# Kernel optimization log

Hardware: AMD Instinct MI355X
Metric: run time of the kernel (lower is better)

## Reference

```python
import jax, jax.numpy as jnp
import numpy as np

B, HGRID, WGRID = 4, 32, 32
L = 1 + HGRID * WGRID          # cls token + spatial tokens
INPUT_DIM = 512
HEAD_DIM = 512
N_HEAD = 8
QKV_DIM = HEAD_DIM * N_HEAD    # 4096


def pos_embed_2d(h, w, C, dtype):
    """Standard 2D sinusoidal positional embedding, shape (h*w, C)."""
    d = C // 4
    omega = 1.0 / (10000.0 ** (jnp.arange(d, dtype=jnp.float32) / d))
    ey = jnp.arange(h, dtype=jnp.float32)[:, None] * omega      # (h, d)
    ex = jnp.arange(w, dtype=jnp.float32)[:, None] * omega      # (w, d)
    emb_y = jnp.concatenate([jnp.sin(ey), jnp.cos(ey)], -1)     # (h, 2d)
    emb_x = jnp.concatenate([jnp.sin(ex), jnp.cos(ex)], -1)     # (w, 2d)
    emb = jnp.concatenate([
        jnp.broadcast_to(emb_y[:, None, :], (h, w, 2 * d)),
        jnp.broadcast_to(emb_x[None, :, :], (h, w, 2 * d)),
    ], -1)                                                       # (h, w, C)
    return emb.reshape(h * w, C).astype(dtype)


def setup_inputs() -> dict:
    key = jax.random.key(0)
    ks = jax.random.split(key, 16)
    s = 0.02
    inp = {
        "x": jax.random.normal(ks[0], (B, L, INPUT_DIM), dtype=jnp.float32),
        # Q/K/V linear: weight (out, in) as in torch Linear, bias zeros (per _init_bias)
        "Wq": jax.random.normal(ks[1], (QKV_DIM, INPUT_DIM), jnp.float32) * s,
        "bq": jnp.zeros((QKV_DIM,), jnp.float32),
        "Wk": jax.random.normal(ks[2], (QKV_DIM, INPUT_DIM), jnp.float32) * s,
        "bk": jnp.zeros((QKV_DIM,), jnp.float32),
        "Wv": jax.random.normal(ks[3], (QKV_DIM, INPUT_DIM), jnp.float32) * s,
        "bv": jnp.zeros((QKV_DIM,), jnp.float32),
        # 1x1 conv poolers: weight (out_ch, in_ch) = (HEAD_DIM, HEAD_DIM)
        "Wpq": jax.random.normal(ks[4], (HEAD_DIM, HEAD_DIM), jnp.float32) * s,
        "bpq": jax.random.normal(ks[5], (HEAD_DIM,), jnp.float32) * s,
        "Wpk": jax.random.normal(ks[6], (HEAD_DIM, HEAD_DIM), jnp.float32) * s,
        "bpk": jax.random.normal(ks[7], (HEAD_DIM,), jnp.float32) * s,
        "Wpv": jax.random.normal(ks[8], (HEAD_DIM, HEAD_DIM), jnp.float32) * s,
        "bpv": jax.random.normal(ks[9], (HEAD_DIM,), jnp.float32) * s,
        # dispatcher linear: (INPUT_DIM, QKV_DIM)
        "Wd": jax.random.normal(ks[10], (INPUT_DIM, QKV_DIM), jnp.float32) * s,
        "bd": jax.random.normal(ks[11], (INPUT_DIM,), jnp.float32) * s,
        "h": HGRID,
        "w": WGRID,
    }
    return inp


def _pool(t, Wp, bp):
    """AttentionPooler with kernel=1/stride=1: pointwise conv on spatial tokens,
    cls token passed through unchanged. t: (B, n_head, L, head_dim)."""
    cls_tok = t[:, :, :1, :]
    sp = jnp.einsum('bnlc,oc->bnlo', t[:, :, 1:, :], Wp) + bp
    return jnp.concatenate([cls_tok, sp], axis=2)


def reference(x, Wq, bq, Wk, bk, Wv, bv, Wpq, bpq, Wpk, bpk, Wpv, bpv, Wd, bd, h, w):
    Bs, Ls, _ = x.shape

    def proj(Wt, bt):
        y = jnp.einsum('bli,oi->blo', x, Wt) + bt
        return y.reshape(Bs, Ls, N_HEAD, HEAD_DIM).transpose(0, 2, 1, 3)  # (B,nh,L,hd)

    Q = proj(Wq, bq)
    K = proj(Wk, bk)
    V = proj(Wv, bv)

    PQ = _pool(Q, Wpq, bpq)
    PK = _pool(K, Wpk, bpk)
    PV = _pool(V, Wpv, bpv)

    # relative positional encoding added to pooled Q's spatial tokens
    emb = pos_embed_2d(h, w, HEAD_DIM, PQ.dtype)                 # (h*w, hd)
    PQ = jnp.concatenate([PQ[:, :, :1, :], PQ[:, :, 1:, :] + emb], axis=2)

    scale = 1.0 / jnp.sqrt(jnp.asarray(HEAD_DIM, PQ.dtype))
    logits = jnp.einsum('bnqc,bnkc->bnqk', PQ, PK) * scale
    attn = jax.nn.softmax(logits, axis=-1)
    sa = jnp.einsum('bnqk,bnkc->bnqc', attn, PV)

    # skip connection on spatial tokens only (cls row excluded)
    sa = jnp.concatenate([sa[:, :, :1, :], sa[:, :, 1:, :] + Q[:, :, 1:, :]], axis=2)

    stacked = sa.transpose(0, 2, 1, 3).reshape(Bs, Ls, QKV_DIM)
    out = jnp.einsum('blq,oq->blo', stacked, Wd) + bd
    return out
```

## Files before the change

### kernel.cpp

```cpp
#include <hip/hip_runtime.h>


typedef unsigned short u16;
typedef __attribute__((ext_vector_type(8))) short short8;
typedef __attribute__((ext_vector_type(4))) float floatx4;
typedef __attribute__((ext_vector_type(4))) unsigned short us4;

__device__ __forceinline__ u16 f2bf(float f) {
  union { float f; unsigned u; } x; x.f = f;
  unsigned r = (x.u + 0x7fffu + ((x.u >> 16) & 1u)) >> 16;
  return (u16)r;
}
__device__ __forceinline__ float bf2f(u16 u) {
  union { unsigned u; float f; } x; x.u = ((unsigned)u) << 16;
  return x.f;
}

__device__ __forceinline__ void gld_lds16(const void* g, void* l) {
  __builtin_amdgcn_global_load_lds(
      (const __attribute__((address_space(1))) void*)g,
      (__attribute__((address_space(3))) void*)l, 16, 0, 0);
}

struct CvtArgs { const float* src[8]; u16* dst[8]; int n4[8]; };

__global__ __launch_bounds__(256) void cvt_all(CvtArgs a, int total4, float* __restrict__ e) {
  int t = blockIdx.x * 256 + threadIdx.x;
  if (t >= total4) {
    int et = (t - total4) * 4;
    if (et >= 1024 * 512) return;
#pragma unroll
    for (int u = 0; u < 4; ++u) {
      int idx = et + u;
      int c = idx & 511, sp = idx >> 9;
      int y = sp >> 5, xg = sp & 31;
      int j = c & 127, seg = c >> 7;
      float omega = expf(-(float)j * (9.210340371976184f / 128.f));
      float arg = (float)((seg < 2) ? y : xg) * omega;
      e[idx] = (seg & 1) ? cosf(arg) : sinf(arg);
    }
    return;
  }
#pragma unroll
  for (int s = 0; s < 8; ++s) {
    if (t < a.n4[s]) {
      const float* sp = a.src[s] + (long)t * 4;
      u16* dp = a.dst[s] + (long)t * 4;
      float4 v = *(const float4*)sp;
      dp[0] = f2bf(v.x); dp[1] = f2bf(v.y); dp[2] = f2bf(v.z); dp[3] = f2bf(v.w);
      return;
    }
    t -= a.n4[s];
  }
}

struct CF {
  const u16* W;
  const u16* Wp;
  const u16* xb;
  const float *bq, *bk, *bv, *bpq, *bpk, *bpv;
  u16 *PQ, *PK, *PVt;
  float* bc;
};

__global__ __launch_bounds__(256) void cls_fold(CF a) {
  int wid = blockIdx.x * 4 + (threadIdx.x >> 6);
  int lane = threadIdx.x & 63;
  if (wid < 12288) {
    int mat = wid >> 12, o2 = wid & 4095, n = o2 >> 9, ch = o2 & 511;
    short8 wv = *(const short8*)(a.W + (long)wid * 512 + lane * 8);
    float wf[8];
#pragma unroll
    for (int e = 0; e < 8; ++e) wf[e] = bf2f((u16)wv[e]);
    float ac[4] = {0.f, 0.f, 0.f, 0.f};
#pragma unroll
    for (int b = 0; b < 4; ++b) {
      short8 xv = *(const short8*)(a.xb + ((long)b * 1025) * 512 + lane * 8);
#pragma unroll
      for (int e = 0; e < 8; ++e) ac[b] += wf[e] * bf2f((u16)xv[e]);
    }
#pragma unroll
    for (int o = 32; o > 0; o >>= 1)
#pragma unroll
      for (int b = 0; b < 4; ++b) ac[b] += __shfl_xor(ac[b], o, 64);
    if (lane == 0) {
      const float* bsrc = (mat == 0) ? a.bq : (mat == 1) ? a.bk : a.bv;
      float bias = bsrc[o2];
#pragma unroll
      for (int b = 0; b < 4; ++b) {
        long bn = b * 8 + n;
        u16 v = f2bf(ac[b] + bias);
        if (mat == 0)      a.PQ[(bn * 1025 + 1024) * 512 + ch] = v;
        else if (mat == 1) a.PK[(bn * 1025 + 1024) * 512 + ch] = v;
        else               a.PVt[(bn * 512 + ch) * 1088 + 1024] = v;
      }
    }
  } else {
    int t2 = wid - 12288;
    int mat = t2 >> 12, o2 = t2 & 4095, n = o2 >> 9, o = o2 & 511;
    const float* bsrc = (mat == 0) ? a.bq : (mat == 1) ? a.bk : a.bv;
    short8 wp = *(const short8*)(a.Wp + (long)mat * 262144 + o * 512 + lane * 8);
    const float* bb = bsrc + n * 512 + lane * 8;
    float4 b0 = *(const float4*)bb;
    float4 b1 = *(const float4*)(bb + 4);
    float bf8[8] = {b0.x, b0.y, b0.z, b0.w, b1.x, b1.y, b1.z, b1.w};
    float s = 0.f;
#pragma unroll
    for (int e = 0; e < 8; ++e) s += bf2f((u16)wp[e]) * bf8[e];
#pragma unroll
    for (int o1 = 32; o1 > 0; o1 >>= 1) s += __shfl_xor(s, o1, 64);
    if (lane == 0) {
      const float* bpp = (mat == 0) ? a.bpq : (mat == 1) ? a.bpk : a.bpv;
      a.bc[t2] = s + bpp[o];
    }
  }
}

__global__ __launch_bounds__(256) void s_edge(const u16* __restrict__ PQ,
                                              const u16* __restrict__ PK,
                                              u16* __restrict__ S, int nh) {
  int flat = blockIdx.x;
  int head, seg;
  if (nh == 32) {
    int xcd = flat & 7, s = flat >> 3;
    head = xcd + 8 * (s >> 3);
    seg = s & 7;
  } else {
    head = flat >> 3;
    seg = flat & 7;
  }
  const u16* pq = PQ + (long)head * 1025 * 512;
  const u16* pk = PK + (long)head * 1025 * 512;
  u16* sh = S + (long)head * 1025 * 1088;
#pragma unroll
  for (int i = 0; i < 2; ++i) {
    int local = i * 256 + (int)threadIdx.x;
    if (local >= 257) continue;
    int e = seg * 257 + local;
    if (e >= 2049) continue;
    int q, kv;
    if (e < 1025) { q = 1024; kv = e; }
    else { q = e - 1025; kv = 1024; }
    const u16* a = pq + (long)q * 512;
    const u16* b = pk + (long)kv * 512;
    float acc = 0.f;
    for (int k8 = 0; k8 < 64; ++k8) {
      short8 av = *(const short8*)(a + k8 * 8);
      short8 bv = *(const short8*)(b + k8 * 8);
#pragma unroll
      for (int u = 0; u < 8; ++u) acc += bf2f((u16)av[u]) * bf2f((u16)bv[u]);
    }
    sh[(long)q * 1088 + kv] = f2bf(acc * 0.04419417382415922f);
  }
}

__global__ __launch_bounds__(256) void softmax_rows(u16* __restrict__ S) {
  int flat = blockIdx.x;
  int xcd = flat & 7, s0 = flat >> 3;
  int zi = s0 / 257, blk = s0 - zi * 257;
  int head = xcd + 8 * zi;
  int wv = threadIdx.x >> 6, lane = threadIdx.x & 63;
  int row_i = blk * 4 + wv;
  if (row_i > 1024) return;
  u16* row = S + ((long)head * 1025 + row_i) * 1088;
  float v[16];
  float mx = -1e30f;
#pragma unroll
  for (int i = 0; i < 4; ++i) {
    us4 p = *(const us4*)(row + i * 256 + lane * 4);
#pragma unroll
    for (int e = 0; e < 4; ++e) { v[i * 4 + e] = bf2f(p[e]); mx = fmaxf(mx, v[i * 4 + e]); }
  }
  float e1024 = (lane == 0) ? bf2f(row[1024]) : -1e30f;
  mx = fmaxf(mx, e1024);
  for (int o = 32; o > 0; o >>= 1) mx = fmaxf(mx, __shfl_xor(mx, o, 64));
  float s = 0.f;
#pragma unroll
  for (int i = 0; i < 16; ++i) { v[i] = __expf(v[i] - mx); s += v[i]; }
  e1024 = (lane == 0) ? __expf(e1024 - mx) : 0.f;
  s += e1024;
  for (int o = 32; o > 0; o >>= 1) s += __shfl_xor(s, o, 64);
  float inv = 1.0f / s;
#pragma unroll
  for (int i = 0; i < 4; ++i) {
    us4 q;
#pragma unroll
    for (int e = 0; e < 4; ++e) q[e] = f2bf(v[i * 4 + e] * inv);
    *(us4*)(row + i * 256 + lane * 4) = q;
  }
  if (lane < 16) {
    us4 q;
#pragma unroll
    for (int e = 0; e < 4; ++e) q[e] = 0;
    if (lane == 0) q[0] = f2bf(e1024 * inv);
    *(us4*)(row + 1024 + lane * 4) = q;
  }
}

__global__ __launch_bounds__(256) void reduce2(const float* __restrict__ part,
                                               const float* __restrict__ bd,
                                               float* __restrict__ out) {
  int t = blockIdx.x * 256 + threadIdx.x;
  long i = (long)t * 4;
  const long STR = 4100ll * 512;
  float4 a = *(const float4*)(part + i);
  float4 b = *(const float4*)(part + i + STR);
  float4 bb = *(const float4*)(bd + (int)(i & 511));
  float4 r;
  r.x = a.x + b.x + bb.x;
  r.y = a.y + b.y + bb.y;
  r.z = a.z + b.z + bb.z;
  r.w = a.w + b.w + bb.w;
  *(float4*)(out + i) = r;
}

struct GP {
  const u16* A; const u16* A2; const u16* B; const u16* B2;
  const float* c0; const float* c1; const float* c2;
  const float* emb; const u16* resid;
  u16* o0; u16* o1; u16* o2;
  u16* p0; u16* p1; u16* p2;
  float* of; int bz0;
};

template <int MODE>
__global__ __launch_bounds__(256) void gemm_bt(GP g) {
  constexpr int KLEN = (MODE == 5) ? 2048 : ((MODE == 4) ? 1088 : 512);
  constexpr int KITER = KLEN / 64;
  __shared__ u16 smem[16384];
  u16* As = smem;
  u16* Bs = smem + 8192;
  const int tid = threadIdx.x;
  const int lane = tid & 63;
  const int wv = tid >> 6;
  const int wr = wv >> 1, wc = wv & 1;
  const int ccol = lane & 15;
  const int rgrp = lane >> 4;

  int mt, nt, bz, mh = 0;
  if constexpr (MODE == 3 || MODE == 4) {
    constexpr int PER = (MODE == 3) ? 64 : 36;
    constexpr int NTW = (MODE == 3) ? 8 : 4;
    int flat = blockIdx.x;
    int xcd = flat & 7, s = flat >> 3;
    bz = xcd + 8 * (s / PER);
    int tile = s % PER;
    mt = tile / NTW;
    nt = tile % NTW;
  } else if constexpr (MODE == 2) {
    int flat = blockIdx.x;
    int xcd = flat & 7, s = flat >> 3;
    bz = 0;
    mt = xcd * 4 + (s >> 5);
    nt = s & 31;
  } else if constexpr (MODE == 6) {
    int flat = blockIdx.x;
    mh = flat >> 4;
    int tile = flat & 15;
    mt = tile >> 2; nt = tile & 3; bz = 0;
  } else {
    mt = blockIdx.y; nt = blockIdx.x; bz = blockIdx.z;
  }
  const int gbz = g.bz0 + bz;

  const u16* Ap = g.A;
  const u16* Bp = g.B;
  if constexpr (MODE == 0) {
    if (nt >= 64) Bp = g.B2;
  }

  int a_row[4], b_row[4], kx[4];
#pragma unroll
  for (int c = 0; c < 4; ++c) {
    int idx = c * 256 + tid;
    int row = idx >> 3;
    kx[c] = ((idx & 7) ^ (row & 7)) * 8;
    {
      int r = mt * 128 + row;
      int off;
      if constexpr (MODE == 0 || MODE == 2) { off = ((r >> 10) * 1025 + 1 + (r & 1023)) * 512; }
      else if constexpr (MODE == 3) { off = gbz * (1025 * 512) + r * 512; }
      else if constexpr (MODE == 4) { r = r < 1024 ? r : 1024; off = bz * (1025 * 1088) + r * 1088; }
      else if constexpr (MODE == 6) { off = (mh >> 3) * 262144 + r * 512; }
      else { r = r < 4099 ? r : 4099; off = r * 4096; }
      a_row[c] = off;
    }
    {
      int off;
      if constexpr (MODE == 6) {
        int rb = idx >> 4, s2 = idx & 15;
        int cg = (s2 - ((rb >> 3) << 1)) & 15;
        off = mh * 262144 + rb * 512 + nt * 128 + cg * 8;
      } else {
        int r = nt * 128 + row;
        if constexpr (MODE == 0) { off = ((nt >= 64) ? (r - 8192) : r) * 512; }
        else if constexpr (MODE == 3) { off = gbz * (1025 * 512) + r * 512; }
        else if constexpr (MODE == 4) { off = gbz * (512 * 1088) + r * 1088; }
        else if constexpr (MODE == 5) { off = r * 4096; }
        else { off = r * 512; }
      }
      b_row[c] = off;
    }
  }

  floatx4 acc[4][4];
  {
    float binit[4] = {0.f, 0.f, 0.f, 0.f};
    if constexpr (MODE == 0) {
      int sec = nt >> 5;
      const float* bs = (sec < 2) ? (g.c0 + sec * 4096) : g.c1;
#pragma unroll
      for (int j = 0; j < 4; ++j) binit[j] = bs[(nt & 31) * 128 + wc * 64 + j * 16 + ccol];
    }
    if constexpr (MODE == 2) {
#pragma unroll
      for (int j = 0; j < 4; ++j) binit[j] = g.c0[nt * 128 + wc * 64 + j * 16 + ccol];
    }
#pragma unroll
    for (int i = 0; i < 4; ++i)
#pragma unroll
      for (int j = 0; j < 4; ++j)
#pragma unroll
        for (int rr = 0; rr < 4; ++rr) acc[i][j][rr] = binit[j];
  }

  const int kbase = (MODE == 5) ? bz * 2048 : 0;
  const int l15 = lane & 15;
  const int lq = lane >> 4;
  const int l7 = lane & 7;

  for (int kt = 0; kt < KITER; ++kt) {
    const int k0 = kbase + kt * 64;
#pragma unroll
    for (int c = 0; c < 4; ++c)
      gld_lds16(Ap + a_row[c] + k0 + kx[c], (char*)As + (c * 256 + wv * 64) * 16);
#pragma unroll
    for (int c = 0; c < 4; ++c) {
      if constexpr (MODE == 6)
        gld_lds16(Bp + b_row[c] + k0 * 512, (char*)Bs + (c * 256 + wv * 64) * 16);
      else
        gld_lds16(Bp + b_row[c] + k0 + kx[c], (char*)Bs + (c * 256 + wv * 64) * 16);
    }
    __syncthreads();
#pragma unroll
    for (int ks = 0; ks < 2; ++ks) {
      const int ch = ((ks * 4 + lq) ^ l7) * 8;
      short8 af[4], bfr[4];
#pragma unroll
      for (int i = 0; i < 4; ++i)
        af[i] = *(const short8*)(As + (wr * 64 + i * 16 + l15) * 64 + ch);
      if constexpr (MODE == 6) {
#pragma unroll
        for (int j = 0; j < 4; ++j) {
          int ro = ((wc * 64 + j * 16 + l15) + ((ks * 4 + lq) << 4)) & 127;
          const u16* bp2 = Bs + (ks * 32 + lq * 8) * 128 + ro;
          short8 tv;
#pragma unroll
          for (int e = 0; e < 8; ++e) tv[e] = (short)bp2[e * 128];
          bfr[j] = tv;
        }
      } else {
#pragma unroll
        for (int j = 0; j < 4; ++j)
          bfr[j] = *(const short8*)(Bs + (wc * 64 + j * 16 + l15) * 64 + ch);
      }
#pragma unroll
      for (int i = 0; i < 4; ++i)
#pragma unroll
        for (int j = 0; j < 4; ++j)
          acc[i][j] = __builtin_amdgcn_mfma_f32_16x16x32_bf16(af[i], bfr[j], acc[i][j], 0, 0, 0);
    }
    __syncthreads();
  }

  if constexpr (MODE == 2) {
#pragma unroll
    for (int i = 0; i < 4; ++i)
#pragma unroll
      for (int j = 0; j < 4; ++j)
#pragma unroll
        for (int rr = 0; rr < 4; ++rr) {
          int lr2 = wc * 64 + j * 16 + ccol;
          int lc2 = wr * 64 + i * 16 + rgrp * 4 + rr;
          smem[lr2 * 128 + (lc2 ^ ((lr2 & 15) << 3))] = f2bf(acc[i][j][rr]);
        }
    __syncthreads();
    {
      int b = mt >> 3, sp0 = (mt & 7) * 128;
      int n = nt >> 2, ch0 = (nt & 3) * 128;
      long bn = b * 8 + n;
#pragma unroll
      for (int q = 0; q < 8; ++q) {
        int cid = q * 256 + tid;
        int r = cid >> 4;
        int c = cid & 15;
        int pc = c ^ (r & 15);
        short8 val = *(const short8*)(smem + r * 128 + pc * 8);
        *(short8*)(g.o0 + (bn * 512 + ch0 + r) * 1088 + sp0 + c * 8) = val;
      }
    }
  } else if constexpr (MODE == 0 || MODE == 3 || MODE == 4 || MODE == 6) {
#pragma unroll
    for (int i = 0; i < 4; ++i)
#pragma unroll
      for (int j = 0; j < 4; ++j)
#pragma unroll
        for (int rr = 0; rr < 4; ++rr) {
          int lr = wr * 64 + i * 16 + rgrp * 4 + rr;
          int lc = wc * 64 + j * 16 + ccol;
          float v = acc[i][j][rr];
          if constexpr (MODE == 3) v *= 0.04419417382415922f;
          smem[lr * 128 + (lc ^ (rgrp << 4))] = f2bf(v);
        }
    __syncthreads();
#pragma unroll
    for (int q = 0; q < 8; ++q) {
      int cid = q * 256 + tid;
      int r = cid >> 4;
      int c = cid & 15;
      int pc = c ^ ((((unsigned)r >> 2) & 3) << 1);
      short8 val = *(const short8*)(smem + r * 128 + pc * 8);
      int grow = mt * 128 + r;
      if constexpr (MODE == 0) {
        const int sec = nt >> 5;
        int b = grow >> 10, sp = grow & 1023;
        int gcol = (nt & 31) * 128 + c * 8;
        int n = gcol >> 9, ch2 = gcol & 511;
        long bn = b * 8 + n;
        if (sec == 0) {
          const float* ep = g.emb + sp * 512 + ch2;
          float4 e0 = *(const float4*)ep;
          float4 e1 = *(const float4*)(ep + 4);
          float ee[8] = {e0.x, e0.y, e0.z, e0.w, e1.x, e1.y, e1.z, e1.w};
          short8 outv;
#pragma unroll
          for (int e = 0; e < 8; ++e) outv[e] = (short)f2bf(bf2f((u16)val[e]) + ee[e]);
          *(short8*)(g.o0 + (bn * 1025 + sp) * 512 + ch2) = outv;
        } else if (sec == 1) {
          *(short8*)(g.o1 + (bn * 1025 + sp) * 512 + ch2) = val;
        } else {
          *(short8*)(g.o2 + (bn * 1025 + 1 + sp) * 512 + ch2) = val;
        }
      } else if constexpr (MODE == 3) {
        *(short8*)(g.o0 + ((long)bz * 1025 + grow) * 1088 + nt * 128 + c * 8) = val;
      } else if constexpr (MODE == 6) {
        *(short8*)(g.o0 + ((long)(mh * 512) + grow) * 512 + nt * 128 + c * 8) = val;
      } else {
        if (grow <= 1024) {
          int gcol0 = nt * 128 + c * 8;
          short8 outv = val;
          int l = (grow == 1024) ? 0 : grow + 1;
          if (grow < 1024) {
            short8 rs = *(const short8*)(g.resid + ((long)gbz * 1025 + l) * 512 + gcol0);
#pragma unroll
            for (int e = 0; e < 8; ++e)
              outv[e] = (short)f2bf(bf2f((u16)val[e]) + bf2f((u16)rs[e]));
          }
          int b = gbz >> 3, n = gbz & 7;
          *(short8*)(g.o0 + (((long)b * 1025 + l) * 8 + n) * 512 + gcol0) = outv;
        }
      }
    }
  } else {
#pragma unroll
    for (int i = 0; i < 4; ++i) {
#pragma unroll
      for (int j = 0; j < 4; ++j) {
        const int gcol = nt * 128 + wc * 64 + j * 16 + ccol;
#pragma unroll
        for (int rr = 0; rr < 4; ++rr) {
          const int grow = mt * 128 + wr * 64 + i * 16 + rgrp * 4 + rr;
          if (grow < 4100)
            g.of[((long)bz * 4100 + grow) * 512 + gcol] = acc[i][j][rr];
        }
      }
    }
  }
}

extern "C" void kernel_launch(void* const* d_in, const int* in_sizes, int n_in,
                              void* d_out, int out_size, void* d_ws, size_t ws_size,
                              hipStream_t stream) {
  const float* x   = (const float*)d_in[0];
  const float* Wq  = (const float*)d_in[1];
  const float* bq  = (const float*)d_in[2];
  const float* Wk  = (const float*)d_in[3];
  const float* bk  = (const float*)d_in[4];
  const float* Wv  = (const float*)d_in[5];
  const float* bv  = (const float*)d_in[6];
  const float* Wpq = (const float*)d_in[7];
  const float* bpq = (const float*)d_in[8];
  const float* Wpk = (const float*)d_in[9];
  const float* bpk = (const float*)d_in[10];
  const float* Wpv = (const float*)d_in[11];
  const float* bpv = (const float*)d_in[12];
  const float* Wd  = (const float*)d_in[13];
  const float* bd  = (const float*)d_in[14];
  float* out = (float*)d_out;

  char* ws = (char*)d_ws;
  size_t off = 0;
  auto alloc = [&](size_t bytes) {
    char* p = ws + off;
    off += (bytes + 255) & ~(size_t)255;
    return p;
  };
  u16* Wpqb = (u16*)alloc(512ull * 512 * 2);
  u16* Wpkb = (u16*)alloc(512ull * 512 * 2);
  u16* Wpvb = (u16*)alloc(512ull * 512 * 2);
  u16* Wdb  = (u16*)alloc(4096ull * 512 * 2);
  u16* Q    = (u16*)alloc(32ull * 1025 * 512 * 2);
  u16* PQ   = (u16*)alloc(32ull * 1025 * 512 * 2);
  u16* PK   = (u16*)alloc(32ull * 1025 * 512 * 2);
  u16* PVt  = (u16*)alloc(32ull * 512 * 1088 * 2);
  size_t s_off = off;
  u16* xb   = (u16*)alloc(4100ull * 512 * 2);
  u16* Wqb  = (u16*)alloc(4096ull * 512 * 2);
  u16* Wkb  = (u16*)alloc(4096ull * 512 * 2);
  u16* Wvb  = (u16*)alloc(4096ull * 512 * 2);
  u16* Wc   = (u16*)alloc(3ull * 4096 * 512 * 2);
  float* bc = (float*)alloc(3ull * 4096 * 4);
  float* embp = (float*)alloc(1024ull * 512 * 4);
  size_t fixed_need = off;
  u16* S = (u16*)(ws + s_off);
  float* part = (float*)PQ;
  (void)in_sizes; (void)n_in; (void)out_size; (void)Wkb; (void)Wvb;
  (void)Wpkb; (void)Wpvb;

  const size_t sbytes = 1025ull * 1088 * 2;
  size_t need1 = s_off + 32ull * sbytes;
  size_t need2 = s_off + 16ull * sbytes;
  size_t stk4_off = s_off + ((8ull * sbytes + 255) & ~(size_t)255);
  size_t need4 = stk4_off + 4100ull * 4096 * 2;
  int nchunk;
  u16* stk;
  if (ws_size >= need1)      { nchunk = 1; stk = PK; }
  else if (ws_size >= need2 && ws_size >= fixed_need) { nchunk = 2; stk = PK; }
  else if (ws_size >= need4 && ws_size >= fixed_need) {
    nchunk = 4; stk = (u16*)(ws + stk4_off);
  } else return;
  if (nchunk == 2) {
    size_t stk2_off = s_off + ((16ull * sbytes + 255) & ~(size_t)255);
    if (ws_size >= stk2_off + 4100ull * 4096 * 2) stk = (u16*)(ws + stk2_off);
    else {
      nchunk = 4;
      if (ws_size >= need4) stk = (u16*)(ws + stk4_off);
      else return;
    }
  }
  int hpc = 32 / nchunk;

  CvtArgs ca;
  ca.src[0] = x;   ca.dst[0] = xb;   ca.n4[0] = 4100 * 512 / 4;
  ca.src[1] = Wq;  ca.dst[1] = Wqb;  ca.n4[1] = 4096 * 512 / 4;
  ca.src[2] = Wk;  ca.dst[2] = Wkb;  ca.n4[2] = 4096 * 512 / 4;
  ca.src[3] = Wv;  ca.dst[3] = Wvb;  ca.n4[3] = 4096 * 512 / 4;
  ca.src[4] = Wpq; ca.dst[4] = Wpqb; ca.n4[4] = 512 * 512 / 4;
  ca.src[5] = Wpk; ca.dst[5] = Wpkb; ca.n4[5] = 512 * 512 / 4;
  ca.src[6] = Wpv; ca.dst[6] = Wpvb; ca.n4[6] = 512 * 512 / 4;
  ca.src[7] = Wd;  ca.dst[7] = Wdb;  ca.n4[7] = 512 * 4096 / 4;
  int total4 = 0;
  for (int s = 0; s < 8; ++s) total4 += ca.n4[s];
  int grid1 = (total4 + 1024 * 512 / 4 + 255) / 256;
  cvt_all<<<grid1, 256, 0, stream>>>(ca, total4, embp);

  {
    GP g = {};
    g.A = Wpqb; g.B = Wqb; g.o0 = Wc;
    gemm_bt<6><<<dim3(384, 1, 1), 256, 0, stream>>>(g);
  }
  {
    CF cf;
    cf.W = Wqb; cf.Wp = Wpqb; cf.xb = xb;
    cf.bq = bq; cf.bk = bk; cf.bv = bv;
    cf.bpq = bpq; cf.bpk = bpk; cf.bpv = bpv;
    cf.PQ = PQ; cf.PK = PK; cf.PVt = PVt; cf.bc = bc;
    cls_fold<<<6144, 256, 0, stream>>>(cf);
  }

  {
    GP g = {};
    g.A = xb; g.B = Wc; g.B2 = Wqb;
    g.c0 = bc; g.c1 = bq; g.emb = embp;
    g.o0 = PQ; g.o1 = PK; g.o2 = Q;
    gemm_bt<0><<<dim3(96, 32, 1), 256, 0, stream>>>(g);
  }
  {
    GP g = {};
    g.A = xb; g.B = Wc + 8192 * 512; g.c0 = bc + 8192; g.o0 = PVt;
    gemm_bt<2><<<dim3(1024, 1, 1), 256, 0, stream>>>(g);
  }

  for (int c = 0; c < nchunk; ++c) {
    GP g3 = {}; g3.A = PQ; g3.B = PK; g3.o0 = S; g3.bz0 = c * hpc;
    gemm_bt<3><<<dim3(64 * hpc, 1, 1), 256, 0, stream>>>(g3);
    s_edge<<<hpc * 8, 256, 0, stream>>>(
        PQ + (long)c * hpc * 1025 * 512, PK + (long)c * hpc * 1025 * 512, S, hpc);
    softmax_rows<<<257 * hpc, 256, 0, stream>>>(S);
    GP g4 = {}; g4.A = S; g4.B = PVt; g4.resid = Q; g4.o0 = stk; g4.bz0 = c * hpc;
    gemm_bt<4><<<dim3(36 * hpc, 1, 1), 256, 0, stream>>>(g4);
  }

  {
    GP g = {}; g.A = stk; g.B = Wdb; g.of = part;
    gemm_bt<5><<<dim3(4, 33, 2), 256, 0, stream>>>(g);
  }
  reduce2<<<(4100 * 512 / 4 + 255) / 256, 256, 0, stream>>>(part, bd, out);
}
```

Measured before the change: 429.1 us.

## Fold Q skip connection through dispatcher weight as precomputed x·(Wd·Wq) term

Instead of materialising Q (B×8×1025×512) in the projection GEMM and adding it as a residual in the attention-output GEMM, the skip term is folded algebraically: Wd·Wq is precomputed as a 512×512 matrix and multiplied directly with x. A bias term Wd·bq is also folded into the final bias for spatial rows. This removes a third of the projection GEMM output writes and the residual reads, at the cost of a small extra GEMM, an fp32 residual buffer, and a different rounding path. The final K-split also changes from 2 to 4 partial sums, so the reduction kernel reads four partials.

Result: slower. 505.6 us (+17.8%).

```diff
diff --git a/kernel.cpp b/kernel.cpp
--- a/kernel.cpp
+++ b/kernel.cpp
@@ -57,10 +57,12 @@
 struct CF {
   const u16* W;
   const u16* Wp;
+  const u16* Wdbp;
   const u16* xb;
-  const float *bq, *bk, *bv, *bpq, *bpk, *bpv;
+  const float *bq, *bk, *bv, *bpq, *bpk, *bpv, *bd;
   u16 *PQ, *PK, *PVt;
   float* bc;
+  float* bdq;
 };
 
 __global__ __launch_bounds__(256) void cls_fold(CF a) {
@@ -95,7 +97,7 @@
         else               a.PVt[(bn * 512 + ch) * 1088 + 1024] = v;
       }
     }
-  } else {
+  } else if (wid < 24576) {
     int t2 = wid - 12288;
     int mat = t2 >> 12, o2 = t2 & 4095, n = o2 >> 9, o = o2 & 511;
     const float* bsrc = (mat == 0) ? a.bq : (mat == 1) ? a.bk : a.bv;
@@ -113,6 +115,21 @@
       const float* bpp = (mat == 0) ? a.bpq : (mat == 1) ? a.bpk : a.bpv;
       a.bc[t2] = s + bpp[o];
     }
+  } else {
+    int o = wid - 24576;
+    float s = 0.f;
+    for (int c8 = 0; c8 < 8; ++c8) {
+      int base = c8 * 512 + lane * 8;
+      short8 wv = *(const short8*)(a.Wdbp + (long)o * 4096 + base);
+      float4 b0 = *(const float4*)(a.bq + base);
+      float4 b1 = *(const float4*)(a.bq + base + 4);
+      float bf8[8] = {b0.x, b0.y, b0.z, b0.w, b1.x, b1.y, b1.z, b1.w};
+#pragma unroll
+      for (int e = 0; e < 8; ++e) s += bf2f((u16)wv[e]) * bf8[e];
+    }
+#pragma unroll
+    for (int o1 = 32; o1 > 0; o1 >>= 1) s += __shfl_xor(s, o1, 64);
+    if (lane == 0) a.bdq[o] = a.bd[o] + s;
   }
 }
 
@@ -197,20 +214,35 @@
   }
 }
 
-__global__ __launch_bounds__(256) void reduce2(const float* __restrict__ part,
+__global__ __launch_bounds__(256) void reduce3(const float* __restrict__ part,
+                                               const float* __restrict__ xres,
                                                const float* __restrict__ bd,
+                                               const float* __restrict__ bdq,
                                                float* __restrict__ out) {
   int t = blockIdx.x * 256 + threadIdx.x;
   long i = (long)t * 4;
   const long STR = 4100ll * 512;
-  float4 a = *(const float4*)(part + i);
-  float4 b = *(const float4*)(part + i + STR);
-  float4 bb = *(const float4*)(bd + (int)(i & 511));
+  float4 a0 = *(const float4*)(part + i);
+  float4 a1 = *(const float4*)(part + i + STR);
+  float4 a2 = *(const float4*)(part + i + 2 * STR);
+  float4 a3 = *(const float4*)(part + i + 3 * STR);
+  int row = (int)(i >> 9);
+  int l = row % 1025;
+  int ch = (int)(i & 511);
   float4 r;
-  r.x = a.x + b.x + bb.x;
-  r.y = a.y + b.y + bb.y;
-  r.z = a.z + b.z + bb.z;
-  r.w = a.w + b.w + bb.w;
+  r.x = a0.x + a1.x + a2.x + a3.x;
+  r.y = a0.y + a1.y + a2.y + a3.y;
+  r.z = a0.z + a1.z + a2.z + a3.z;
+  r.w = a0.w + a1.w + a2.w + a3.w;
+  if (l > 0) {
+    float4 xr = *(const float4*)(xres + i);
+    float4 bb = *(const float4*)(bdq + ch);
+    r.x += xr.x + bb.x; r.y += xr.y + bb.y;
+    r.z += xr.z + bb.z; r.w += xr.w + bb.w;
+  } else {
+    float4 bb = *(const float4*)(bd + ch);
+    r.x += bb.x; r.y += bb.y; r.z += bb.z; r.w += bb.w;
+  }
   *(float4*)(out + i) = r;
 }
 
@@ -225,7 +257,7 @@
 
 template <int MODE>
 __global__ __launch_bounds__(256) void gemm_bt(GP g) {
-  constexpr int KLEN = (MODE == 5) ? 2048 : ((MODE == 4) ? 1088 : 512);
+  constexpr int KLEN = (MODE == 5) ? 1024 : ((MODE == 4) ? 1088 : ((MODE == 7) ? 4096 : 512));
   constexpr int KITER = KLEN / 64;
   __shared__ u16 smem[16384];
   u16* As = smem;
@@ -258,6 +290,8 @@
     mh = flat >> 4;
     int tile = flat & 15;
     mt = tile >> 2; nt = tile & 3; bz = 0;
+  } else if constexpr (MODE == 7 || MODE == 8) {
+    mt = blockIdx.x >> 2; nt = blockIdx.x & 3; bz = 0;
   } else {
     mt = blockIdx.y; nt = blockIdx.x; bz = blockIdx.z;
   }
@@ -265,9 +299,6 @@
 
   const u16* Ap = g.A;
   const u16* Bp = g.B;
-  if constexpr (MODE == 0) {
-    if (nt >= 64) Bp = g.B2;
-  }
 
   int a_row[4], b_row[4], kx[4];
 #pragma unroll
@@ -278,23 +309,23 @@
     {
       int r = mt * 128 + row;
       int off;
-      if constexpr (MODE == 0 || MODE == 2) { off = ((r >> 10) * 1025 + 1 + (r & 1023)) * 512; }
+      if constexpr (MODE == 0 || MODE == 2 || MODE == 8) { off = ((r >> 10) * 1025 + 1 + (r & 1023)) * 512; }
       else if constexpr (MODE == 3) { off = gbz * (1025 * 512) + r * 512; }
       else if constexpr (MODE == 4) { r = r < 1024 ? r : 1024; off = bz * (1025 * 1088) + r * 1088; }
       else if constexpr (MODE == 6) { off = (mh >> 3) * 262144 + r * 512; }
+      else if constexpr (MODE == 7) { off = r * 4096; }
       else { r = r < 4099 ? r : 4099; off = r * 4096; }
       a_row[c] = off;
     }
     {
       int off;
-      if constexpr (MODE == 6) {
+      if constexpr (MODE == 6 || MODE == 7) {
         int rb = idx >> 4, s2 = idx & 15;
         int cg = (s2 - ((rb >> 3) << 1)) & 15;
-        off = mh * 262144 + rb * 512 + nt * 128 + cg * 8;
+        off = ((MODE == 6) ? mh * 262144 : 0) + rb * 512 + nt * 128 + cg * 8;
       } else {
         int r = nt * 128 + row;
-        if constexpr (MODE == 0) { off = ((nt >= 64) ? (r - 8192) : r) * 512; }
-        else if constexpr (MODE == 3) { off = gbz * (1025 * 512) + r * 512; }
+        if constexpr (MODE == 3) { off = gbz * (1025 * 512) + r * 512; }
         else if constexpr (MODE == 4) { off = gbz * (512 * 1088) + r * 1088; }
         else if constexpr (MODE == 5) { off = r * 4096; }
         else { off = r * 512; }
@@ -308,7 +339,7 @@
     float binit[4] = {0.f, 0.f, 0.f, 0.f};
     if constexpr (MODE == 0) {
       int sec = nt >> 5;
-      const float* bs = (sec < 2) ? (g.c0 + sec * 4096) : g.c1;
+      const float* bs = g.c0 + sec * 4096;
 #pragma unroll
       for (int j = 0; j < 4; ++j) binit[j] = bs[(nt & 31) * 128 + wc * 64 + j * 16 + ccol];
     }
@@ -324,7 +355,7 @@
         for (int rr = 0; rr < 4; ++rr) acc[i][j][rr] = binit[j];
   }
 
-  const int kbase = (MODE == 5) ? bz * 2048 : 0;
+  const int kbase = (MODE == 5) ? bz * 1024 : 0;
   const int l15 = lane & 15;
   const int lq = lane >> 4;
   const int l7 = lane & 7;
@@ -336,7 +367,7 @@
       gld_lds16(Ap + a_row[c] + k0 + kx[c], (char*)As + (c * 256 + wv * 64) * 16);
 #pragma unroll
     for (int c = 0; c < 4; ++c) {
-      if constexpr (MODE == 6)
+      if constexpr (MODE == 6 || MODE == 7)
         gld_lds16(Bp + b_row[c] + k0 * 512, (char*)Bs + (c * 256 + wv * 64) * 16);
       else
         gld_lds16(Bp + b_row[c] + k0 + kx[c], (char*)Bs + (c * 256 + wv * 64) * 16);
@@ -349,7 +380,7 @@
 #pragma unroll
       for (int i = 0; i < 4; ++i)
         af[i] = *(const short8*)(As + (wr * 64 + i * 16 + l15) * 64 + ch);
-      if constexpr (MODE == 6) {
+      if constexpr (MODE == 6 || MODE == 7) {
 #pragma unroll
         for (int j = 0; j < 4; ++j) {
           int ro = ((wc * 64 + j * 16 + l15) + ((ks * 4 + lq) << 4)) & 127;
@@ -399,7 +430,7 @@
         *(short8*)(g.o0 + (bn * 512 + ch0 + r) * 1088 + sp0 + c * 8) = val;
       }
     }
-  } else if constexpr (MODE == 0 || MODE == 3 || MODE == 4 || MODE == 6) {
+  } else if constexpr (MODE == 0 || MODE == 3 || MODE == 4 || MODE == 6 || MODE == 7) {
 #pragma unroll
     for (int i = 0; i < 4; ++i)
 #pragma unroll
@@ -436,28 +467,33 @@
 #pragma unroll
           for (int e = 0; e < 8; ++e) outv[e] = (short)f2bf(bf2f((u16)val[e]) + ee[e]);
           *(short8*)(g.o0 + (bn * 1025 + sp) * 512 + ch2) = outv;
-        } else if (sec == 1) {
+        } else {
           *(short8*)(g.o1 + (bn * 1025 + sp) * 512 + ch2) = val;
-        } else {
-          *(short8*)(g.o2 + (bn * 1025 + 1 + sp) * 512 + ch2) = val;
         }
       } else if constexpr (MODE == 3) {
         *(short8*)(g.o0 + ((long)bz * 1025 + grow) * 1088 + nt * 128 + c * 8) = val;
-      } else if constexpr (MODE == 6) {
+      } else if constexpr (MODE == 6 || MODE == 7) {
         *(short8*)(g.o0 + ((long)(mh * 512) + grow) * 512 + nt * 128 + c * 8) = val;
       } else {
         if (grow <= 1024) {
           int gcol0 = nt * 128 + c * 8;
-          short8 outv = val;
           int l = (grow == 1024) ? 0 : grow + 1;
-          if (grow < 1024) {
-            short8 rs = *(const short8*)(g.resid + ((long)gbz * 1025 + l) * 512 + gcol0);
-#pragma unroll
-            for (int e = 0; e < 8; ++e)
-              outv[e] = (short)f2bf(bf2f((u16)val[e]) + bf2f((u16)rs[e]));
-          }
           int b = gbz >> 3, n = gbz & 7;
-          *(short8*)(g.o0 + (((long)b * 1025 + l) * 8 + n) * 512 + gcol0) = outv;
+          *(short8*)(g.o0 + (((long)b * 1025 + l) * 8 + n) * 512 + gcol0) = val;
+        }
+      }
+    }
+  } else if constexpr (MODE == 8) {
+#pragma unroll
+    for (int i = 0; i < 4; ++i) {
+#pragma unroll
+      for (int j = 0; j < 4; ++j) {
+        const int gcol = nt * 128 + wc * 64 + j * 16 + ccol;
+#pragma unroll
+        for (int rr = 0; rr < 4; ++rr) {
+          const int grow = mt * 128 + wr * 64 + i * 16 + rgrp * 4 + rr;
+          const int orow = (grow >> 10) * 1025 + 1 + (grow & 1023);
+          g.of[(long)orow * 512 + gcol] = acc[i][j][rr];
         }
       }
     }
@@ -509,10 +545,11 @@
   u16* Wpkb = (u16*)alloc(512ull * 512 * 2);
   u16* Wpvb = (u16*)alloc(512ull * 512 * 2);
   u16* Wdb  = (u16*)alloc(4096ull * 512 * 2);
-  u16* Q    = (u16*)alloc(32ull * 1025 * 512 * 2);
   u16* PQ   = (u16*)alloc(32ull * 1025 * 512 * 2);
   u16* PK   = (u16*)alloc(32ull * 1025 * 512 * 2);
   u16* PVt  = (u16*)alloc(32ull * 512 * 1088 * 2);
+  float* xres = (float*)alloc(4100ull * 512 * 4);
+  float* bdq  = (float*)alloc(512ull * 4);
   size_t s_off = off;
   u16* xb   = (u16*)alloc(4100ull * 512 * 2);
   u16* Wqb  = (u16*)alloc(4096ull * 512 * 2);
@@ -521,6 +558,7 @@
   u16* Wc   = (u16*)alloc(3ull * 4096 * 512 * 2);
   float* bc = (float*)alloc(3ull * 4096 * 4);
   float* embp = (float*)alloc(1024ull * 512 * 4);
+  u16* Wdq  = (u16*)alloc(512ull * 512 * 2);
   size_t fixed_need = off;
   u16* S = (u16*)(ws + s_off);
   float* part = (float*)PQ;
@@ -570,25 +608,35 @@
     gemm_bt<6><<<dim3(384, 1, 1), 256, 0, stream>>>(g);
   }
   {
+    GP g = {};
+    g.A = Wdb; g.B = Wqb; g.o0 = Wdq;
+    gemm_bt<7><<<dim3(16, 1, 1), 256, 0, stream>>>(g);
+  }
+  {
     CF cf;
-    cf.W = Wqb; cf.Wp = Wpqb; cf.xb = xb;
+    cf.W = Wqb; cf.Wp = Wpqb; cf.Wdbp = Wdb; cf.xb = xb;
     cf.bq = bq; cf.bk = bk; cf.bv = bv;
-    cf.bpq = bpq; cf.bpk = bpk; cf.bpv = bpv;
-    cf.PQ = PQ; cf.PK = PK; cf.PVt = PVt; cf.bc = bc;
-    cls_fold<<<6144, 256, 0, stream>>>(cf);
+    cf.bpq = bpq; cf.bpk = bpk; cf.bpv = bpv; cf.bd = bd;
+    cf.PQ = PQ; cf.PK = PK; cf.PVt = PVt; cf.bc = bc; cf.bdq = bdq;
+    cls_fold<<<6272, 256, 0, stream>>>(cf);
   }
 
   {
     GP g = {};
-    g.A = xb; g.B = Wc; g.B2 = Wqb;
-    g.c0 = bc; g.c1 = bq; g.emb = embp;
-    g.o0 = PQ; g.o1 = PK; g.o2 = Q;
-    gemm_bt<0><<<dim3(96, 32, 1), 256, 0, stream>>>(g);
+    g.A = xb; g.B = Wc;
+    g.c0 = bc; g.emb = embp;
+    g.o0 = PQ; g.o1 = PK;
+    gemm_bt<0><<<dim3(64, 32, 1), 256, 0, stream>>>(g);
   }
   {
     GP g = {};
     g.A = xb; g.B = Wc + 8192 * 512; g.c0 = bc + 8192; g.o0 = PVt;
     gemm_bt<2><<<dim3(1024, 1, 1), 256, 0, stream>>>(g);
+  }
+  {
+    GP g = {};
+    g.A = xb; g.B = Wdq; g.of = xres;
+    gemm_bt<8><<<dim3(128, 1, 1), 256, 0, stream>>>(g);
   }
 
   for (int c = 0; c < nchunk; ++c) {
@@ -597,13 +645,13 @@
     s_edge<<<hpc * 8, 256, 0, stream>>>(
         PQ + (long)c * hpc * 1025 * 512, PK + (long)c * hpc * 1025 * 512, S, hpc);
     softmax_rows<<<257 * hpc, 256, 0, stream>>>(S);
-    GP g4 = {}; g4.A = S; g4.B = PVt; g4.resid = Q; g4.o0 = stk; g4.bz0 = c * hpc;
+    GP g4 = {}; g4.A = S; g4.B = PVt; g4.o0 = stk; g4.bz0 = c * hpc;
     gemm_bt<4><<<dim3(36 * hpc, 1, 1), 256, 0, stream>>>(g4);
   }
 
   {
     GP g = {}; g.A = stk; g.B = Wdb; g.of = part;
-    gemm_bt<5><<<dim3(4, 33, 2), 256, 0, stream>>>(g);
-  }
-  reduce2<<<(4100 * 512 / 4 + 255) / 256, 256, 0, stream>>>(part, bd, out);
-}
+    gemm_bt<5><<<dim3(4, 33, 4), 256, 0, stream>>>(g);
+  }
+  reduce3<<<(4100 * 512 / 4 + 255) / 256, 256, 0, stream>>>(part, xres, bd, bdq, out);
+}
```
